# Kernel optimization log

Hardware: AMD Instinct MI355X
Metric: run time of the kernel (lower is better)

The kernel has to match this reference:

```python
import jax, jax.numpy as jnp
import numpy as np

D = 256      # d_model
H = 8        # n_heads
HD = D // H  # head_dim = 32
P = 16       # point dim per head


def setup_inputs() -> dict:
    key = jax.random.key(0)
    ks = jax.random.split(key, 12)
    B, S = 2, 2048
    w = lambda k, shape: jax.random.normal(k, shape, jnp.float32) * 0.02
    return {
        "seq_repr": jax.random.normal(ks[0], (B, S, D), jnp.float32),
        "coords": jax.random.normal(ks[1], (B, S, 3, 3), jnp.float32),
        "frames": jax.random.normal(ks[2], (B, S, 4), jnp.float32),
        "mask": jnp.ones((B, S), jnp.int32),
        "Wq": w(ks[3], (D, D)), "bq": jnp.zeros((D,), jnp.float32),
        "Wk": w(ks[4], (D, D)), "bk": jnp.zeros((D,), jnp.float32),
        "Wv": w(ks[5], (D, D)), "bv": jnp.zeros((D,), jnp.float32),
        "Wpq": w(ks[6], (3, H * P)), "bpq": jnp.zeros((H * P,), jnp.float32),
        "Wpk": w(ks[7], (3, H * P)), "bpk": jnp.zeros((H * P,), jnp.float32),
        "Wo": w(ks[8], (D, D)), "bo": jnp.zeros((D,), jnp.float32),
        "Wpo": w(ks[9], (H * P, 3)), "bpo": jnp.zeros((3,), jnp.float32),
        "attn_bias": jnp.zeros((H,), jnp.float32),
    }


def reference(seq_repr, coords, frames, mask, Wq, bq, Wk, bk, Wv, bv,
              Wpq, bpq, Wpk, bpk, Wo, bo, Wpo, bpo, attn_bias):
    B, S, _ = seq_repr.shape
    q = (seq_repr @ Wq + bq).reshape(B, S, H, HD)
    k = (seq_repr @ Wk + bk).reshape(B, S, H, HD)
    v = (seq_repr @ Wv + bv).reshape(B, S, H, HD)

    rep = coords[..., 1, :]                                  # [B,S,3] representative atom
    pq = (rep @ Wpq + bpq).reshape(B, S, H, P)
    pk = (rep @ Wpk + bpk).reshape(B, S, H, P)

    scale = 1.0 / np.sqrt(HD)
    scores = (jnp.einsum('bihd,bjhd->bhij', q, k) * scale
              + jnp.einsum('bihp,bjhp->bhij', pq, pk) * 0.25  # 1/sqrt(16)
              + attn_bias[None, :, None, None])

    mask2d = (mask[:, :, None] * mask[:, None, :])[:, None]  # [B,1,S,S]
    scores = jnp.where(mask2d == 0, jnp.float32(-1e9), scores)

    w = jax.nn.softmax(scores, axis=-1)                      # [B,H,S,S]

    seq_ctx = jnp.einsum('bhij,bjhd->bihd', w, v).reshape(B, S, D)
    pt_ctx = jnp.einsum('bhij,bjhp->bihp', w, pq).reshape(B, S, H * P)

    seq_out = seq_ctx @ Wo + bo                              # [B,S,D]
    point_out = pt_ctx @ Wpo + bpo                           # [B,S,3]
    return (seq_out, point_out)
```

## Files before the change

kernel.cpp:

```cpp
#include <hip/hip_runtime.h>
#include <hip/hip_bf16.h>

#define D_ 256
#define H_ 8
#define B_ 2
#define S_ 2048
#define MTOT 4096
#define AUGQ 64
#define NBH 16
#define KPAD 72
#define NSPLIT 4
#define NJ 8
#define LOG2E 1.4426950408889634f

typedef __attribute__((ext_vector_type(8))) short short8;
typedef __attribute__((ext_vector_type(4))) short short4v;
typedef __attribute__((ext_vector_type(4))) float f32x4;

static __device__ __forceinline__ short bf16_of(float f) {
  union { __hip_bfloat16 h; short s; } u;
  u.h = __float2bfloat16(f);
  return u.s;
}
static __device__ __forceinline__ float f_of_bf16(short s) {
  union { float f; unsigned int u; } u;
  u.u = ((unsigned int)(unsigned short)s) << 16;
  return u.f;
}

static __device__ __forceinline__ int sinv64(int c) {
  return (((((c >> 2) & 1) << 1) | ((c >> 5) & 1)) << 4) + (((c >> 3) & 3) << 2) + (c & 3);
}


__global__ __launch_bounds__(256) void prep_all(
    const float* __restrict__ Wq, const float* __restrict__ Wk,
    const float* __restrict__ Wv, const float* __restrict__ Wo,
    const float* __restrict__ X, const float* __restrict__ coords,
    const int* __restrict__ mask,
    const float* __restrict__ Wpq, const float* __restrict__ bpq,
    const float* __restrict__ Wpk, const float* __restrict__ bpk,
    short* __restrict__ Wqkv_t, short* __restrict__ Wo_t,
    short* __restrict__ Xb,
    short* __restrict__ Qa, short* __restrict__ Ka, short* __restrict__ VaT) {
  int bid = blockIdx.x, tid = threadIdx.x;

  if (bid < 64) {
    __shared__ short T[64][72];
    const float* src;
    short* dst;
    int k0, n0g;
    if (bid < 48) {
      int nt = bid >> 2;
      k0 = (bid & 3) * 64;
      n0g = nt * 64;
      src = (n0g < 256) ? Wq : (n0g < 512 ? Wk : Wv);
      dst = Wqkv_t;
    } else {
      int t2 = bid - 48;
      k0 = (t2 & 3) * 64;
      n0g = (t2 >> 2) * 64;
      src = Wo;
      dst = Wo_t;
    }
    int ncol = n0g & 255;
    int rr = tid >> 4, cc = (tid & 15) * 4;
#pragma unroll
    for (int i = 0; i < 4; i++) {
      int r = rr + i * 16;
      f32x4 v = *reinterpret_cast<const f32x4*>(&src[(size_t)(k0 + r) * 256 + ncol + cc]);
      T[cc + 0][r] = bf16_of(v[0]);
      T[cc + 1][r] = bf16_of(v[1]);
      T[cc + 2][r] = bf16_of(v[2]);
      T[cc + 3][r] = bf16_of(v[3]);
    }
    __syncthreads();
    int n = tid >> 2, kk = (tid & 3) * 16;
    *reinterpret_cast<short8*>(&dst[(size_t)(n0g + n) * 256 + k0 + kk]) =
        *reinterpret_cast<const short8*>(&T[n][kk]);
    *reinterpret_cast<short8*>(&dst[(size_t)(n0g + n) * 256 + k0 + kk + 8]) =
        *reinterpret_cast<const short8*>(&T[n][kk + 8]);
    return;
  }

  if (bid < 576) {
    size_t i = (size_t)(bid - 64) * 2048 + tid * 8;
    f32x4 v0 = *reinterpret_cast<const f32x4*>(&X[i]);
    f32x4 v1 = *reinterpret_cast<const f32x4*>(&X[i + 4]);
    short8 o;
    o[0] = bf16_of(v0[0]); o[1] = bf16_of(v0[1]); o[2] = bf16_of(v0[2]); o[3] = bf16_of(v0[3]);
    o[4] = bf16_of(v1[0]); o[5] = bf16_of(v1[1]); o[6] = bf16_of(v1[2]); o[7] = bf16_of(v1[3]);
    *reinterpret_cast<short8*>(&Xb[i]) = o;
    return;
  }

  if (bid < 704) {
    int idx = (bid - 576) * 256 + tid;
    int m = idx >> 3, h = idx & 7;
    int b = m >> 11, s = m & 2047;
    float r0 = coords[m * 9 + 3], r1 = coords[m * 9 + 4], r2 = coords[m * 9 + 5];
    size_t base = ((size_t)(b * 8 + h) * S_ + s) * AUGQ;
    short8 pqv[2], pkv[2];
#pragma unroll
    for (int c = 0; c < 2; c++)
#pragma unroll
      for (int i = 0; i < 8; i++) {
        int j = h * 16 + c * 8 + i;
        float pq = r0 * Wpq[j] + r1 * Wpq[128 + j] + r2 * Wpq[256 + j] + bpq[j];
        float pk = r0 * Wpk[j] + r1 * Wpk[128 + j] + r2 * Wpk[256 + j] + bpk[j];
        pqv[c][i] = bf16_of(pq * LOG2E);
        pkv[c][i] = bf16_of(pk * 0.25f);
      }
    short8 padq = {};
    padq[0] = bf16_of(LOG2E);
    short8 padk = {};
    padk[0] = mask[m] ? (short)0 : bf16_of(-1e9f);
    short8 z = {};
    *reinterpret_cast<short8*>(&Qa[base + 32]) = pqv[0];
    *reinterpret_cast<short8*>(&Qa[base + 40]) = pqv[1];
    *reinterpret_cast<short8*>(&Qa[base + 48]) = padq;
    *reinterpret_cast<short8*>(&Qa[base + 56]) = z;
    *reinterpret_cast<short8*>(&Ka[base + 32]) = pkv[0];
    *reinterpret_cast<short8*>(&Ka[base + 40]) = pkv[1];
    *reinterpret_cast<short8*>(&Ka[base + 48]) = padk;
    *reinterpret_cast<short8*>(&Ka[base + 56]) = z;
    return;
  }

  {
    int idx = (bid - 704) * 256 + tid;
    int s8 = idx & 255, p = (idx >> 8) & 15, bh = idx >> 12;
    int b = bh >> 3, h = bh & 7, j = h * 16 + p;
    float w0 = Wpq[j], w1 = Wpq[128 + j], w2 = Wpq[256 + j], bb = bpq[j];
    short8 o;
#pragma unroll
    for (int i = 0; i < 8; i++) {
      int c = (s8 & 7) * 8 + i;
      int m = b * 2048 + (s8 >> 3) * 64 + sinv64(c);
      o[i] = bf16_of(coords[m * 9 + 3] * w0 + coords[m * 9 + 4] * w1 +
                     coords[m * 9 + 5] * w2 + bb);
    }
    *reinterpret_cast<short8*>(&VaT[((size_t)bh * 48 + 32 + p) * S_ + s8 * 8]) = o;
  }
}


__global__ __launch_bounds__(256) void qkv_gemm(
    const short* __restrict__ Xb, const short* __restrict__ Wt,
    const float* __restrict__ bq, const float* __restrict__ bk, const float* __restrict__ bv,
    short* __restrict__ Qa, short* __restrict__ Ka, short* __restrict__ VaT) {
  __shared__ __align__(16) short As[64 * 136];
  __shared__ __align__(16) short Bs[64 * 136];
  int m0 = blockIdx.x * 64, n0 = blockIdx.y * 64;
  int tid = threadIdx.x, lane = tid & 63, w = tid >> 6;
  int t = lane & 15, g = lane >> 4, kf = g * 8;
  int wr = (w >> 1) * 32, wc = (w & 1) * 32;
  f32x4 acc[2][2] = {};
  int srow = tid >> 2, skc = (tid & 3) * 32;
  for (int ph = 0; ph < 2; ph++) {
    int k0 = ph * 128;
    __syncthreads();
    {
      const uint4* xsrc = reinterpret_cast<const uint4*>(&Xb[(size_t)(m0 + srow) * 256 + k0 + skc]);
      const uint4* wsrc = reinterpret_cast<const uint4*>(&Wt[(size_t)(n0 + srow) * 256 + k0 + skc]);
#pragma unroll
      for (int i = 0; i < 4; i++)
        *reinterpret_cast<uint4*>(&As[srow * 136 + skc + i * 8]) = xsrc[i];
#pragma unroll
      for (int i = 0; i < 4; i++)
        *reinterpret_cast<uint4*>(&Bs[srow * 136 + skc + i * 8]) = wsrc[i];
    }
    __syncthreads();
#pragma unroll
    for (int kk = 0; kk < 4; kk++) {
      short8 a[2], bb[2];
#pragma unroll
      for (int i = 0; i < 2; i++)
        a[i] = *reinterpret_cast<const short8*>(&As[(wr + i * 16 + t) * 136 + kk * 32 + kf]);
#pragma unroll
      for (int jj = 0; jj < 2; jj++)
        bb[jj] = *reinterpret_cast<const short8*>(&Bs[(wc + jj * 16 + t) * 136 + kk * 32 + kf]);
#pragma unroll
      for (int i = 0; i < 2; i++)
#pragma unroll
        for (int jj = 0; jj < 2; jj++)
          acc[i][jj] = __builtin_amdgcn_mfma_f32_16x16x32_bf16(a[i], bb[jj], acc[i][jj], 0, 0, 0);
    }
  }
  __syncthreads();
  short* Cs = As;
  const float scale = 0.17677669529663687f * LOG2E;
  int b = m0 >> 11, sbase = m0 & 2047;
#pragma unroll
  for (int i = 0; i < 2; i++)
#pragma unroll
    for (int jj = 0; jj < 2; jj++)
#pragma unroll
      for (int r = 0; r < 4; r++) {
        int rl = wr + i * 16 + g * 4 + r;
        int cl = wc + jj * 16 + t;
        int n = n0 + cl;
        float v = acc[i][jj][r];
        if (n < 256) v = (v + bq[n]) * scale;
        else if (n < 512) v = v + bk[n - 256];
        else v = v + bv[n - 512];
        Cs[rl * 72 + cl] = bf16_of(v);
      }
  __syncthreads();
  if (n0 < 512) {
#pragma unroll
    for (int i2 = 0; i2 < 2; i2++) {
      int task = tid + i2 * 256;
      int row = task >> 3, c = task & 7;
      int n = n0 + c * 8;
      short* dst = (n < 256) ? Qa : Ka;
      int nn = n & 255;
      int hh = nn >> 5, d = nn & 31;
      *reinterpret_cast<short8*>(&dst[((size_t)(b * 8 + hh) * S_ + sbase + row) * AUGQ + d]) =
          *reinterpret_cast<const short8*>(&Cs[row * 72 + c * 8]);
    }
  } else {
    int hv0 = (n0 - 512) >> 5;
#pragma unroll
    for (int i2 = 0; i2 < 2; i2++) {
      int task = tid + i2 * 256;
      int fl = task >> 3, s8 = task & 7;
      short8 o;
#pragma unroll
      for (int i = 0; i < 8; i++) o[i] = Cs[sinv64(s8 * 8 + i) * 72 + fl];
      int hh = hv0 + (fl >> 5), d = fl & 31;
      *reinterpret_cast<short8*>(&VaT[((size_t)(b * 8 + hh) * 48 + d) * S_ + sbase + s8 * 8]) = o;
    }
  }
}


__global__ __launch_bounds__(256, 4) void attn(
    const short* __restrict__ Qa, const short* __restrict__ Ka,
    const short* __restrict__ VaT,
    short* __restrict__ Ctx, float* __restrict__ AccL) {
  __shared__ __align__(16) char smem[32256];

  int bid = blockIdx.x;
  int xcd = bid & 7, slot = bid >> 3;
  int gidx = xcd * 8 + (slot >> 4);
  int it = slot & 15;
  int split = gidx & 3;
  int bhv = gidx >> 2;

  int tid = threadIdx.x, lane = tid & 63, w = tid >> 6;
  int t = lane & 15, g = lane >> 4, kf = g * 8;
  int q0w = it * 128 + w * 32;
  size_t bh = (size_t)bhv * S_;

  short8 aq[2][2];
#pragma unroll
  for (int g2 = 0; g2 < 2; g2++)
#pragma unroll
    for (int c = 0; c < 2; c++)
      aq[g2][c] = *reinterpret_cast<const short8*>(
          &Qa[(bh + q0w + g2 * 16 + t) * AUGQ + c * 32 + kf]);

  short8 onesA = {};
  if (t == 0) {
#pragma unroll
    for (int i = 0; i < 8; i++) onesA[i] = 0x3F80;
  }

  f32x4 OaccA[3] = {}, OaccB[3] = {};
  f32x4 OaccA3 = {}, OaccB3 = {};

  uint4 kreg0, kreg1, vreg0, vreg1;
  int srow = tid >> 3, sko = (tid & 7) * 8;
  const int jt0 = split * NJ;

  auto issue = [&](int jt) {
    const uint4* ks = reinterpret_cast<const uint4*>(&Ka[(bh + jt * 64) * AUGQ]);
    kreg0 = ks[tid];
    kreg1 = ks[tid + 256];
    size_t vb = (size_t)bhv * 48 * S_ + jt * 64;
    vreg0 = *reinterpret_cast<const uint4*>(&VaT[vb + (size_t)srow * S_ + sko]);
    if (tid < 128)
      vreg1 = *reinterpret_cast<const uint4*>(&VaT[vb + (size_t)(srow + 32) * S_ + sko]);
  };
  auto commit = [&](int buf) {
    short* Kd = (short*)(smem + buf * 9216);
    short* Vd = (short*)(smem + 18432 + buf * 6912);
    *reinterpret_cast<uint4*>(&Kd[srow * KPAD + sko]) = kreg0;
    *reinterpret_cast<uint4*>(&Kd[(srow + 32) * KPAD + sko]) = kreg1;
    *reinterpret_cast<uint4*>(&Vd[srow * KPAD + sko]) = vreg0;
    if (tid < 128)
      *reinterpret_cast<uint4*>(&Vd[(srow + 32) * KPAD + sko]) = vreg1;
  };

  issue(jt0);
  commit(0);
  __syncthreads();

  for (int j = 0; j < NJ; j++) {
    int cur = j & 1;
    if (j + 1 < NJ) issue(jt0 + j + 1);
    const short* Kc = (const short*)(smem + cur * 9216);
    const short* Vc = (const short*)(smem + 18432 + cur * 6912);
    short8 pA[2], pB[2];
#pragma unroll
    for (int sub = 0; sub < 4; sub++) {
      short8 ka0 = *reinterpret_cast<const short8*>(&Kc[(sub * 16 + t) * KPAD + kf]);
      short8 ka1 = *reinterpret_cast<const short8*>(&Kc[(sub * 16 + t) * KPAD + 32 + kf]);
      f32x4 sA = {}, sB = {};
      sA = __builtin_amdgcn_mfma_f32_16x16x32_bf16(ka0, aq[0][0], sA, 0, 0, 0);
      sA = __builtin_amdgcn_mfma_f32_16x16x32_bf16(ka1, aq[0][1], sA, 0, 0, 0);
      sB = __builtin_amdgcn_mfma_f32_16x16x32_bf16(ka0, aq[1][0], sB, 0, 0, 0);
      sB = __builtin_amdgcn_mfma_f32_16x16x32_bf16(ka1, aq[1][1], sB, 0, 0, 0);
      float a0 = exp2f(sA[0]), a1 = exp2f(sA[1]), a2 = exp2f(sA[2]), a3 = exp2f(sA[3]);
      float b0 = exp2f(sB[0]), b1 = exp2f(sB[1]), b2 = exp2f(sB[2]), b3 = exp2f(sB[3]);
      int ww = sub & 1, off = (sub >> 1) * 4;
      pA[ww][off + 0] = bf16_of(a0); pA[ww][off + 1] = bf16_of(a1);
      pA[ww][off + 2] = bf16_of(a2); pA[ww][off + 3] = bf16_of(a3);
      pB[ww][off + 0] = bf16_of(b0); pB[ww][off + 1] = bf16_of(b1);
      pB[ww][off + 2] = bf16_of(b2); pB[ww][off + 3] = bf16_of(b3);
    }
    if (j + 1 < NJ) commit(cur ^ 1);
    __builtin_amdgcn_s_setprio(1);
#pragma unroll
    for (int tt = 0; tt < 3; tt++) {
#pragma unroll
      for (int w2 = 0; w2 < 2; w2++) {
        short8 va = *reinterpret_cast<const short8*>(&Vc[(tt * 16 + t) * KPAD + w2 * 32 + kf]);
        OaccA[tt] = __builtin_amdgcn_mfma_f32_16x16x32_bf16(va, pA[w2], OaccA[tt], 0, 0, 0);
        OaccB[tt] = __builtin_amdgcn_mfma_f32_16x16x32_bf16(va, pB[w2], OaccB[tt], 0, 0, 0);
      }
    }
#pragma unroll
    for (int w2 = 0; w2 < 2; w2++) {
      OaccA3 = __builtin_amdgcn_mfma_f32_16x16x32_bf16(onesA, pA[w2], OaccA3, 0, 0, 0);
      OaccB3 = __builtin_amdgcn_mfma_f32_16x16x32_bf16(onesA, pB[w2], OaccB3, 0, 0, 0);
    }
    __builtin_amdgcn_s_setprio(0);
    __syncthreads();
  }

  float* Of = (float*)smem;
#pragma unroll
  for (int tt = 0; tt < 3; tt++)
#pragma unroll
    for (int r = 0; r < 4; r++) {
      Of[(w * 32 + t) * 52 + tt * 16 + g * 4 + r] = OaccA[tt][r];
      Of[(w * 32 + 16 + t) * 52 + tt * 16 + g * 4 + r] = OaccB[tt][r];
    }
  if (lane < 16) {
    size_t lb = (size_t)(split * NBH + bhv) * S_ + q0w + lane;
    AccL[lb] = OaccA3[0];
    AccL[lb + 16] = OaccB3[0];
  }
  __syncthreads();
  short* CtxP = Ctx + (size_t)split * NBH * S_ * 48;
  size_t obase = bh + it * 128;
  for (int task = tid; task < 768; task += 256) {
    int row = task / 6, c8 = task % 6;
    const float* src = &Of[row * 52 + c8 * 8];
    short8 o;
#pragma unroll
    for (int i = 0; i < 8; i++) o[i] = bf16_of(src[i]);
    *reinterpret_cast<short8*>(&CtxP[(obase + row) * 48 + c8 * 8]) = o;
  }
}


__global__ __launch_bounds__(512) void out_gemm(
    const short* __restrict__ Ctx, const float* __restrict__ AccL,
    const short* __restrict__ Wot, const float* __restrict__ bo,
    const float* __restrict__ Wpo, const float* __restrict__ bpo,
    float* __restrict__ Out) {
  const size_t CTXSZ = (size_t)NBH * S_ * 48;
  int m0 = blockIdx.x * 64;
  int tid = threadIdx.x;
  int b = m0 >> 11, sbase = m0 & 2047;

  if (blockIdx.y == 4) {
    int row = tid >> 3, hh = tid & 7;
    int m = m0 + row, s = sbase + row;
    size_t rowO = (size_t)(b * 8 + hh) * S_ + s;
    float l = 0.f;
#pragma unroll
    for (int sp = 0; sp < NSPLIT; sp++) l += AccL[(size_t)sp * NBH * S_ + rowO];
    float inv = 1.0f / l;
    float a0 = 0.f, a1 = 0.f, a2 = 0.f;
#pragma unroll
    for (int half = 0; half < 2; half++) {
      float sum[8] = {};
#pragma unroll
      for (int sp = 0; sp < NSPLIT; sp++) {
        short8 v = *reinterpret_cast<const short8*>(&Ctx[sp * CTXSZ + rowO * 48 + 32 + half * 8]);
#pragma unroll
        for (int c = 0; c < 8; c++) sum[c] += f_of_bf16(v[c]);
      }
#pragma unroll
      for (int c = 0; c < 8; c++) {
        float val = sum[c] * inv;
        int j = hh * 16 + half * 8 + c;
        a0 += val * Wpo[j * 3 + 0];
        a1 += val * Wpo[j * 3 + 1];
        a2 += val * Wpo[j * 3 + 2];
      }
    }
    a0 += __shfl_xor(a0, 1); a0 += __shfl_xor(a0, 2); a0 += __shfl_xor(a0, 4);
    a1 += __shfl_xor(a1, 1); a1 += __shfl_xor(a1, 2); a1 += __shfl_xor(a1, 4);
    a2 += __shfl_xor(a2, 1); a2 += __shfl_xor(a2, 2); a2 += __shfl_xor(a2, 4);
    if (hh == 0) {
      float* po = Out + (size_t)MTOT * 256;
      po[(size_t)m * 3 + 0] = a0 + bpo[0];
      po[(size_t)m * 3 + 1] = a1 + bpo[1];
      po[(size_t)m * 3 + 2] = a2 + bpo[2];
    }
    return;
  }

  __shared__ __align__(16) short As[64 * 136];
  __shared__ __align__(16) short Bs[64 * 136];
  int n0 = blockIdx.y * 64;
  int lane = tid & 63, w = tid >> 6;
  int t = lane & 15, g = lane >> 4, kf = g * 8;
  int wm = w & 3, wn = w >> 2;
  f32x4 acc[2] = {};
  int srow = tid >> 3, skc = (tid & 7) * 16;
  for (int ph = 0; ph < 2; ph++) {
    int k0 = ph * 128;
    __syncthreads();
    {
      int kg = k0 + skc;
      int hh = kg >> 5, d0 = kg & 31;
      size_t rowO = (size_t)(b * 8 + hh) * S_ + sbase + srow;
      float l = 0.f;
#pragma unroll
      for (int sp = 0; sp < NSPLIT; sp++) l += AccL[(size_t)sp * NBH * S_ + rowO];
      float inv = 1.0f / l;
#pragma unroll
      for (int half = 0; half < 2; half++) {
        float sum[8] = {};
#pragma unroll
        for (int sp = 0; sp < NSPLIT; sp++) {
          short8 a = *reinterpret_cast<const short8*>(&Ctx[sp * CTXSZ + rowO * 48 + d0 + half * 8]);
#pragma unroll
          for (int c = 0; c < 8; c++) sum[c] += f_of_bf16(a[c]);
        }
        short8 o;
#pragma unroll
        for (int c = 0; c < 8; c++) o[c] = bf16_of(sum[c] * inv);
        *reinterpret_cast<short8*>(&As[srow * 136 + skc + half * 8]) = o;
      }
      *reinterpret_cast<uint4*>(&Bs[srow * 136 + skc]) =
          *reinterpret_cast<const uint4*>(&Wot[(size_t)(n0 + srow) * 256 + kg]);
      *reinterpret_cast<uint4*>(&Bs[srow * 136 + skc + 8]) =
          *reinterpret_cast<const uint4*>(&Wot[(size_t)(n0 + srow) * 256 + kg + 8]);
    }
    __syncthreads();
#pragma unroll
    for (int kk = 0; kk < 4; kk++) {
      short8 a = *reinterpret_cast<const short8*>(&As[(wm * 16 + t) * 136 + kk * 32 + kf]);
#pragma unroll
      for (int jj = 0; jj < 2; jj++) {
        short8 bb = *reinterpret_cast<const short8*>(&Bs[(wn * 32 + jj * 16 + t) * 136 + kk * 32 + kf]);
        acc[jj] = __builtin_amdgcn_mfma_f32_16x16x32_bf16(a, bb, acc[jj], 0, 0, 0);
      }
    }
  }
#pragma unroll
  for (int jj = 0; jj < 2; jj++)
#pragma unroll
    for (int r = 0; r < 4; r++) {
      int mrow = m0 + wm * 16 + g * 4 + r;
      int n = n0 + wn * 32 + jj * 16 + t;
      Out[(size_t)mrow * 256 + n] = acc[jj][r] + bo[n];
    }
}


extern "C" void kernel_launch(void* const* d_in, const int* in_sizes, int n_in,
                              void* d_out, int out_size, void* d_ws, size_t ws_size,
                              hipStream_t stream) {
  const float* seq    = (const float*)d_in[0];
  const float* coords = (const float*)d_in[1];
  const int*   mask   = (const int*)d_in[3];
  const float* Wq  = (const float*)d_in[4];
  const float* bq  = (const float*)d_in[5];
  const float* Wk  = (const float*)d_in[6];
  const float* bk  = (const float*)d_in[7];
  const float* Wv  = (const float*)d_in[8];
  const float* bv  = (const float*)d_in[9];
  const float* Wpq = (const float*)d_in[10];
  const float* bpq = (const float*)d_in[11];
  const float* Wpk = (const float*)d_in[12];
  const float* bpk = (const float*)d_in[13];
  const float* Wo  = (const float*)d_in[14];
  const float* bo  = (const float*)d_in[15];
  const float* Wpo = (const float*)d_in[16];
  const float* bpo = (const float*)d_in[17];
  float* out = (float*)d_out;

  char* ws = (char*)d_ws;
  short* Wqkv_t = (short*)ws; ws += 768 * 256 * 2;
  short* Wo_t   = (short*)ws; ws += 256 * 256 * 2;
  short* Xb     = (short*)ws; ws += (size_t)MTOT * D_ * 2;
  short* Qa     = (short*)ws; ws += (size_t)NBH * S_ * AUGQ * 2;
  short* Ka     = (short*)ws; ws += (size_t)NBH * S_ * AUGQ * 2;
  short* VaT    = (short*)ws; ws += (size_t)NBH * 48 * S_ * 2;
  short* Ctx    = (short*)ws; ws += (size_t)NSPLIT * NBH * S_ * 48 * 2;
  float* AccL   = (float*)ws; ws += (size_t)NSPLIT * NBH * S_ * 4;

  prep_all<<<960, 256, 0, stream>>>(Wq, Wk, Wv, Wo, seq, coords, mask,
                                    Wpq, bpq, Wpk, bpk,
                                    Wqkv_t, Wo_t, Xb, Qa, Ka, VaT);
  qkv_gemm<<<dim3(64, 12), 256, 0, stream>>>(Xb, Wqkv_t, bq, bk, bv, Qa, Ka, VaT);
  attn<<<1024, 256, 0, stream>>>(Qa, Ka, VaT, Ctx, AccL);
  out_gemm<<<dim3(64, 5), 512, 0, stream>>>(Ctx, AccL, Wo_t, bo, Wpo, bpo, out);
}
```

Before: 59.97 us.

## Fuse four stages into one cooperative persistent kernel with grid syncs

Turns the four kernels (prep, QKV GEMM, attention, output GEMM) into device functions and runs them from a single cooperatively launched kernel of 1024 blocks, separated by grid-wide barriers. The goal is to drop the launch gaps and tail drain between kernels. The output GEMM is also reshaped from 512-thread blocks with a separate point-output column to 256-thread blocks with wider per-wave N tiles, plus separate blocks for the point output. Risks: grid sync costs, the need for all 1024 blocks to be co-resident (checked via occupancy, with a fallback to separate launches), and larger shared memory that may reduce occupancy.

```diff
diff --git a/kernel.cpp b/kernel.cpp
--- a/kernel.cpp
+++ b/kernel.cpp
@@ -1,5 +1,8 @@
 #include <hip/hip_runtime.h>
+#include <hip/hip_cooperative_groups.h>
 #include <hip/hip_bf16.h>
+
+namespace cg = cooperative_groups;
 
 #define D_ 256
 #define H_ 8
@@ -33,7 +36,7 @@
 }
 
 
-__global__ __launch_bounds__(256) void prep_all(
+static __device__ void prep_body(int bid, int tid, char* smem,
     const float* __restrict__ Wq, const float* __restrict__ Wk,
     const float* __restrict__ Wv, const float* __restrict__ Wo,
     const float* __restrict__ X, const float* __restrict__ coords,
@@ -43,10 +46,8 @@
     short* __restrict__ Wqkv_t, short* __restrict__ Wo_t,
     short* __restrict__ Xb,
     short* __restrict__ Qa, short* __restrict__ Ka, short* __restrict__ VaT) {
-  int bid = blockIdx.x, tid = threadIdx.x;
-
   if (bid < 64) {
-    __shared__ short T[64][72];
+    short* T = (short*)smem;
     const float* src;
     short* dst;
     int k0, n0g;
@@ -69,17 +70,17 @@
     for (int i = 0; i < 4; i++) {
       int r = rr + i * 16;
       f32x4 v = *reinterpret_cast<const f32x4*>(&src[(size_t)(k0 + r) * 256 + ncol + cc]);
-      T[cc + 0][r] = bf16_of(v[0]);
-      T[cc + 1][r] = bf16_of(v[1]);
-      T[cc + 2][r] = bf16_of(v[2]);
-      T[cc + 3][r] = bf16_of(v[3]);
+      T[(cc + 0) * 72 + r] = bf16_of(v[0]);
+      T[(cc + 1) * 72 + r] = bf16_of(v[1]);
+      T[(cc + 2) * 72 + r] = bf16_of(v[2]);
+      T[(cc + 3) * 72 + r] = bf16_of(v[3]);
     }
     __syncthreads();
     int n = tid >> 2, kk = (tid & 3) * 16;
     *reinterpret_cast<short8*>(&dst[(size_t)(n0g + n) * 256 + k0 + kk]) =
-        *reinterpret_cast<const short8*>(&T[n][kk]);
+        *reinterpret_cast<const short8*>(&T[n * 72 + kk]);
     *reinterpret_cast<short8*>(&dst[(size_t)(n0g + n) * 256 + k0 + kk + 8]) =
-        *reinterpret_cast<const short8*>(&T[n][kk + 8]);
+        *reinterpret_cast<const short8*>(&T[n * 72 + kk + 8]);
     return;
   }
 
@@ -144,15 +145,14 @@
   }
 }
 
-
-__global__ __launch_bounds__(256) void qkv_gemm(
+static __device__ void qkv_body(int vb, int tid, char* smem,
     const short* __restrict__ Xb, const short* __restrict__ Wt,
     const float* __restrict__ bq, const float* __restrict__ bk, const float* __restrict__ bv,
     short* __restrict__ Qa, short* __restrict__ Ka, short* __restrict__ VaT) {
-  __shared__ __align__(16) short As[64 * 136];
-  __shared__ __align__(16) short Bs[64 * 136];
-  int m0 = blockIdx.x * 64, n0 = blockIdx.y * 64;
-  int tid = threadIdx.x, lane = tid & 63, w = tid >> 6;
+  short* As = (short*)smem;
+  short* Bs = (short*)(smem + 17408);
+  int m0 = (vb & 63) * 64, n0 = (vb >> 6) * 64;
+  int lane = tid & 63, w = tid >> 6;
   int t = lane & 15, g = lane >> 4, kf = g * 8;
   int wr = (w >> 1) * 32, wc = (w & 1) * 32;
   f32x4 acc[2][2] = {};
@@ -234,21 +234,17 @@
   }
 }
 
-
-__global__ __launch_bounds__(256, 4) void attn(
+static __device__ void attn_body(int vb, int tid, char* smem,
     const short* __restrict__ Qa, const short* __restrict__ Ka,
     const short* __restrict__ VaT,
     short* __restrict__ Ctx, float* __restrict__ AccL) {
-  __shared__ __align__(16) char smem[32256];
-
-  int bid = blockIdx.x;
-  int xcd = bid & 7, slot = bid >> 3;
+  int xcd = vb & 7, slot = vb >> 3;
   int gidx = xcd * 8 + (slot >> 4);
   int it = slot & 15;
   int split = gidx & 3;
   int bhv = gidx >> 2;
 
-  int tid = threadIdx.x, lane = tid & 63, w = tid >> 6;
+  int lane = tid & 63, w = tid >> 6;
   int t = lane & 15, g = lane >> 4, kf = g * 8;
   int q0w = it * 128 + w * 32;
   size_t bh = (size_t)bhv * S_;
@@ -278,10 +274,10 @@
     const uint4* ks = reinterpret_cast<const uint4*>(&Ka[(bh + jt * 64) * AUGQ]);
     kreg0 = ks[tid];
     kreg1 = ks[tid + 256];
-    size_t vb = (size_t)bhv * 48 * S_ + jt * 64;
-    vreg0 = *reinterpret_cast<const uint4*>(&VaT[vb + (size_t)srow * S_ + sko]);
+    size_t vbv = (size_t)bhv * 48 * S_ + jt * 64;
+    vreg0 = *reinterpret_cast<const uint4*>(&VaT[vbv + (size_t)srow * S_ + sko]);
     if (tid < 128)
-      vreg1 = *reinterpret_cast<const uint4*>(&VaT[vb + (size_t)(srow + 32) * S_ + sko]);
+      vreg1 = *reinterpret_cast<const uint4*>(&VaT[vbv + (size_t)(srow + 32) * S_ + sko]);
   };
   auto commit = [&](int buf) {
     short* Kd = (short*)(smem + buf * 9216);
@@ -366,113 +362,174 @@
   }
 }
 
-
-__global__ __launch_bounds__(512) void out_gemm(
+static __device__ void out_body(int vb, int tid, char* smem,
     const short* __restrict__ Ctx, const float* __restrict__ AccL,
     const short* __restrict__ Wot, const float* __restrict__ bo,
     const float* __restrict__ Wpo, const float* __restrict__ bpo,
     float* __restrict__ Out) {
   const size_t CTXSZ = (size_t)NBH * S_ * 48;
-  int m0 = blockIdx.x * 64;
-  int tid = threadIdx.x;
-  int b = m0 >> 11, sbase = m0 & 2047;
-
-  if (blockIdx.y == 4) {
-    int row = tid >> 3, hh = tid & 7;
-    int m = m0 + row, s = sbase + row;
-    size_t rowO = (size_t)(b * 8 + hh) * S_ + s;
-    float l = 0.f;
-#pragma unroll
-    for (int sp = 0; sp < NSPLIT; sp++) l += AccL[(size_t)sp * NBH * S_ + rowO];
-    float inv = 1.0f / l;
-    float a0 = 0.f, a1 = 0.f, a2 = 0.f;
-#pragma unroll
-    for (int half = 0; half < 2; half++) {
-      float sum[8] = {};
-#pragma unroll
-      for (int sp = 0; sp < NSPLIT; sp++) {
-        short8 v = *reinterpret_cast<const short8*>(&Ctx[sp * CTXSZ + rowO * 48 + 32 + half * 8]);
-#pragma unroll
-        for (int c = 0; c < 8; c++) sum[c] += f_of_bf16(v[c]);
-      }
-#pragma unroll
-      for (int c = 0; c < 8; c++) {
-        float val = sum[c] * inv;
-        int j = hh * 16 + half * 8 + c;
-        a0 += val * Wpo[j * 3 + 0];
-        a1 += val * Wpo[j * 3 + 1];
-        a2 += val * Wpo[j * 3 + 2];
-      }
-    }
-    a0 += __shfl_xor(a0, 1); a0 += __shfl_xor(a0, 2); a0 += __shfl_xor(a0, 4);
-    a1 += __shfl_xor(a1, 1); a1 += __shfl_xor(a1, 2); a1 += __shfl_xor(a1, 4);
-    a2 += __shfl_xor(a2, 1); a2 += __shfl_xor(a2, 2); a2 += __shfl_xor(a2, 4);
-    if (hh == 0) {
-      float* po = Out + (size_t)MTOT * 256;
-      po[(size_t)m * 3 + 0] = a0 + bpo[0];
-      po[(size_t)m * 3 + 1] = a1 + bpo[1];
-      po[(size_t)m * 3 + 2] = a2 + bpo[2];
-    }
-    return;
-  }
-
-  __shared__ __align__(16) short As[64 * 136];
-  __shared__ __align__(16) short Bs[64 * 136];
-  int n0 = blockIdx.y * 64;
-  int lane = tid & 63, w = tid >> 6;
-  int t = lane & 15, g = lane >> 4, kf = g * 8;
-  int wm = w & 3, wn = w >> 2;
-  f32x4 acc[2] = {};
-  int srow = tid >> 3, skc = (tid & 7) * 16;
-  for (int ph = 0; ph < 2; ph++) {
-    int k0 = ph * 128;
-    __syncthreads();
-    {
-      int kg = k0 + skc;
-      int hh = kg >> 5, d0 = kg & 31;
-      size_t rowO = (size_t)(b * 8 + hh) * S_ + sbase + srow;
+  if (vb < 256) {
+    int m0 = (vb & 63) * 64, n0 = (vb >> 6) * 64;
+    int b = m0 >> 11, sbase = m0 & 2047;
+    short* As = (short*)smem;
+    short* Bs = (short*)(smem + 17408);
+    int lane = tid & 63, w = tid >> 6;
+    int t = lane & 15, g = lane >> 4, kf = g * 8;
+    f32x4 acc4[4] = {};
+    int srow = tid >> 2, skc = (tid & 3) * 32;
+    for (int ph = 0; ph < 2; ph++) {
+      int k0 = ph * 128;
+      __syncthreads();
+      {
+        int kg = k0 + skc;
+        int hh = kg >> 5;
+        size_t rowO = (size_t)(b * 8 + hh) * S_ + sbase + srow;
+        float l = 0.f;
+#pragma unroll
+        for (int sp = 0; sp < NSPLIT; sp++) l += AccL[(size_t)sp * NBH * S_ + rowO];
+        float inv = 1.0f / l;
+#pragma unroll
+        for (int q8 = 0; q8 < 4; q8++) {
+          float sum[8] = {};
+#pragma unroll
+          for (int sp = 0; sp < NSPLIT; sp++) {
+            short8 a = *reinterpret_cast<const short8*>(&Ctx[sp * CTXSZ + rowO * 48 + q8 * 8]);
+#pragma unroll
+            for (int c = 0; c < 8; c++) sum[c] += f_of_bf16(a[c]);
+          }
+          short8 o;
+#pragma unroll
+          for (int c = 0; c < 8; c++) o[c] = bf16_of(sum[c] * inv);
+          *reinterpret_cast<short8*>(&As[srow * 136 + skc + q8 * 8]) = o;
+        }
+#pragma unroll
+        for (int i = 0; i < 4; i++)
+          *reinterpret_cast<uint4*>(&Bs[srow * 136 + skc + i * 8]) =
+              *reinterpret_cast<const uint4*>(&Wot[(size_t)(n0 + srow) * 256 + kg + i * 8]);
+      }
+      __syncthreads();
+#pragma unroll
+      for (int kk = 0; kk < 4; kk++) {
+        short8 a = *reinterpret_cast<const short8*>(&As[(w * 16 + t) * 136 + kk * 32 + kf]);
+#pragma unroll
+        for (int jj = 0; jj < 4; jj++) {
+          short8 bb = *reinterpret_cast<const short8*>(&Bs[(jj * 16 + t) * 136 + kk * 32 + kf]);
+          acc4[jj] = __builtin_amdgcn_mfma_f32_16x16x32_bf16(a, bb, acc4[jj], 0, 0, 0);
+        }
+      }
+    }
+#pragma unroll
+    for (int jj = 0; jj < 4; jj++)
+#pragma unroll
+      for (int r = 0; r < 4; r++) {
+        int mrow = m0 + w * 16 + g * 4 + r;
+        int n = n0 + jj * 16 + t;
+        Out[(size_t)mrow * 256 + n] = acc4[jj][r] + bo[n];
+      }
+  } else if (vb < 320) {
+    int m0 = (vb - 256) * 64;
+    int b = m0 >> 11, sbase = m0 & 2047;
+#pragma unroll
+    for (int r2 = 0; r2 < 2; r2++) {
+      int row = r2 * 32 + (tid >> 3), hh = tid & 7;
+      int m = m0 + row, s = sbase + row;
+      size_t rowO = (size_t)(b * 8 + hh) * S_ + s;
       float l = 0.f;
 #pragma unroll
       for (int sp = 0; sp < NSPLIT; sp++) l += AccL[(size_t)sp * NBH * S_ + rowO];
       float inv = 1.0f / l;
+      float a0 = 0.f, a1 = 0.f, a2 = 0.f;
 #pragma unroll
       for (int half = 0; half < 2; half++) {
         float sum[8] = {};
 #pragma unroll
         for (int sp = 0; sp < NSPLIT; sp++) {
-          short8 a = *reinterpret_cast<const short8*>(&Ctx[sp * CTXSZ + rowO * 48 + d0 + half * 8]);
-#pragma unroll
-          for (int c = 0; c < 8; c++) sum[c] += f_of_bf16(a[c]);
+          short8 v = *reinterpret_cast<const short8*>(&Ctx[sp * CTXSZ + rowO * 48 + 32 + half * 8]);
+#pragma unroll
+          for (int c = 0; c < 8; c++) sum[c] += f_of_bf16(v[c]);
         }
-        short8 o;
-#pragma unroll
-        for (int c = 0; c < 8; c++) o[c] = bf16_of(sum[c] * inv);
-        *reinterpret_cast<short8*>(&As[srow * 136 + skc + half * 8]) = o;
-      }
-      *reinterpret_cast<uint4*>(&Bs[srow * 136 + skc]) =
-          *reinterpret_cast<const uint4*>(&Wot[(size_t)(n0 + srow) * 256 + kg]);
-      *reinterpret_cast<uint4*>(&Bs[srow * 136 + skc + 8]) =
-          *reinterpret_cast<const uint4*>(&Wot[(size_t)(n0 + srow) * 256 + kg + 8]);
-    }
-    __syncthreads();
-#pragma unroll
-    for (int kk = 0; kk < 4; kk++) {
-      short8 a = *reinterpret_cast<const short8*>(&As[(wm * 16 + t) * 136 + kk * 32 + kf]);
-#pragma unroll
-      for (int jj = 0; jj < 2; jj++) {
-        short8 bb = *reinterpret_cast<const short8*>(&Bs[(wn * 32 + jj * 16 + t) * 136 + kk * 32 + kf]);
-        acc[jj] = __builtin_amdgcn_mfma_f32_16x16x32_bf16(a, bb, acc[jj], 0, 0, 0);
-      }
-    }
-  }
-#pragma unroll
-  for (int jj = 0; jj < 2; jj++)
-#pragma unroll
-    for (int r = 0; r < 4; r++) {
-      int mrow = m0 + wm * 16 + g * 4 + r;
-      int n = n0 + wn * 32 + jj * 16 + t;
-      Out[(size_t)mrow * 256 + n] = acc[jj][r] + bo[n];
-    }
+#pragma unroll
+        for (int c = 0; c < 8; c++) {
+          float val = sum[c] * inv;
+          int j = hh * 16 + half * 8 + c;
+          a0 += val * Wpo[j * 3 + 0];
+          a1 += val * Wpo[j * 3 + 1];
+          a2 += val * Wpo[j * 3 + 2];
+        }
+      }
+      a0 += __shfl_xor(a0, 1); a0 += __shfl_xor(a0, 2); a0 += __shfl_xor(a0, 4);
+      a1 += __shfl_xor(a1, 1); a1 += __shfl_xor(a1, 2); a1 += __shfl_xor(a1, 4);
+      a2 += __shfl_xor(a2, 1); a2 += __shfl_xor(a2, 2); a2 += __shfl_xor(a2, 4);
+      if (hh == 0) {
+        float* po = Out + (size_t)MTOT * 256;
+        po[(size_t)m * 3 + 0] = a0 + bpo[0];
+        po[(size_t)m * 3 + 1] = a1 + bpo[1];
+        po[(size_t)m * 3 + 2] = a2 + bpo[2];
+      }
+    }
+  }
+}
+
+
+__global__ __launch_bounds__(256, 4) void mega(
+    const float* Wq, const float* Wk, const float* Wv, const float* Wo,
+    const float* seq, const float* coords, const int* mask,
+    const float* Wpq, const float* bpq, const float* Wpk, const float* bpk,
+    const float* bq, const float* bk, const float* bv, const float* bo,
+    const float* Wpo, const float* bpo, float* out,
+    short* Wqkv_t, short* Wo_t, short* Xb,
+    short* Qa, short* Ka, short* VaT, short* Ctx, float* AccL) {
+  __shared__ __align__(16) char smem[34816];
+  int bid = blockIdx.x, tid = threadIdx.x;
+
+  if (bid < 960)
+    prep_body(bid, tid, smem, Wq, Wk, Wv, Wo, seq, coords, mask,
+              Wpq, bpq, Wpk, bpk, Wqkv_t, Wo_t, Xb, Qa, Ka, VaT);
+  cg::this_grid().sync();
+
+  if (bid < 768)
+    qkv_body(bid, tid, smem, Xb, Wqkv_t, bq, bk, bv, Qa, Ka, VaT);
+  cg::this_grid().sync();
+
+  attn_body(bid, tid, smem, Qa, Ka, VaT, Ctx, AccL);
+  cg::this_grid().sync();
+
+  if (bid < 320)
+    out_body(bid, tid, smem, Ctx, AccL, Wo_t, bo, Wpo, bpo, out);
+}
+
+
+__global__ __launch_bounds__(256) void prep_k(
+    const float* Wq, const float* Wk, const float* Wv, const float* Wo,
+    const float* seq, const float* coords, const int* mask,
+    const float* Wpq, const float* bpq, const float* Wpk, const float* bpk,
+    short* Wqkv_t, short* Wo_t, short* Xb,
+    short* Qa, short* Ka, short* VaT) {
+  __shared__ __align__(16) char smem[9216];
+  prep_body(blockIdx.x, threadIdx.x, smem, Wq, Wk, Wv, Wo, seq, coords, mask,
+            Wpq, bpq, Wpk, bpk, Wqkv_t, Wo_t, Xb, Qa, Ka, VaT);
+}
+
+__global__ __launch_bounds__(256) void qkv_k(
+    const short* Xb, const short* Wt,
+    const float* bq, const float* bk, const float* bv,
+    short* Qa, short* Ka, short* VaT) {
+  __shared__ __align__(16) char smem[34816];
+  qkv_body(blockIdx.x, threadIdx.x, smem, Xb, Wt, bq, bk, bv, Qa, Ka, VaT);
+}
+
+__global__ __launch_bounds__(256, 4) void attn_k(
+    const short* Qa, const short* Ka, const short* VaT,
+    short* Ctx, float* AccL) {
+  __shared__ __align__(16) char smem[32256];
+  attn_body(blockIdx.x, threadIdx.x, smem, Qa, Ka, VaT, Ctx, AccL);
+}
+
+__global__ __launch_bounds__(256) void out_k(
+    const short* Ctx, const float* AccL, const short* Wot,
+    const float* bo, const float* Wpo, const float* bpo, float* Out) {
+  __shared__ __align__(16) char smem[34816];
+  out_body(blockIdx.x, threadIdx.x, smem, Ctx, AccL, Wot, bo, Wpo, bpo, Out);
 }
 
 
@@ -508,10 +565,28 @@
   short* Ctx    = (short*)ws; ws += (size_t)NSPLIT * NBH * S_ * 48 * 2;
   float* AccL   = (float*)ws; ws += (size_t)NSPLIT * NBH * S_ * 4;
 
-  prep_all<<<960, 256, 0, stream>>>(Wq, Wk, Wv, Wo, seq, coords, mask,
-                                    Wpq, bpq, Wpk, bpk,
-                                    Wqkv_t, Wo_t, Xb, Qa, Ka, VaT);
-  qkv_gemm<<<dim3(64, 12), 256, 0, stream>>>(Xb, Wqkv_t, bq, bk, bv, Qa, Ka, VaT);
-  attn<<<1024, 256, 0, stream>>>(Qa, Ka, VaT, Ctx, AccL);
-  out_gemm<<<dim3(64, 5), 512, 0, stream>>>(Ctx, AccL, Wo_t, bo, Wpo, bpo, out);
-}
+  int coopBlocks = 0;
+  hipError_t qerr = hipOccupancyMaxActiveBlocksPerMultiprocessor(&coopBlocks, mega, 256, 0);
+  bool useCoop = (qerr == hipSuccess && coopBlocks >= 4);
+
+  if (useCoop) {
+    void* kargs[] = {
+      (void*)&Wq, (void*)&Wk, (void*)&Wv, (void*)&Wo,
+      (void*)&seq, (void*)&coords, (void*)&mask,
+      (void*)&Wpq, (void*)&bpq, (void*)&Wpk, (void*)&bpk,
+      (void*)&bq, (void*)&bk, (void*)&bv, (void*)&bo,
+      (void*)&Wpo, (void*)&bpo, (void*)&out,
+      (void*)&Wqkv_t, (void*)&Wo_t, (void*)&Xb,
+      (void*)&Qa, (void*)&Ka, (void*)&VaT, (void*)&Ctx, (void*)&AccL
+    };
+    hipError_t lerr = hipLaunchCooperativeKernel((const void*)mega, dim3(1024), dim3(256),
+                                                 kargs, 0, stream);
+    if (lerr == hipSuccess) return;
+  }
+
+  prep_k<<<960, 256, 0, stream>>>(Wq, Wk, Wv, Wo, seq, coords, mask,
+                                  Wpq, bpq, Wpk, bpk, Wqkv_t, Wo_t, Xb, Qa, Ka, VaT);
+  qkv_k<<<768, 256, 0, stream>>>(Xb, Wqkv_t, bq, bk, bv, Qa, Ka, VaT);
+  attn_k<<<1024, 256, 0, stream>>>(Qa, Ka, VaT, Ctx, AccL);
+  out_k<<<320, 256, 0, stream>>>(Ctx, AccL, Wo_t, bo, Wpo, bpo, out);
+}
```

New measurement: 66.76 us. 11.3% more time.
